# Kernel tuning notes

Hardware: AMD Instinct MI355X
Metric: run time of the kernel (lower is better)

## Reference

```python
import jax, jax.numpy as jnp
import numpy as np
from functools import partial

CONF_THRESH = 0.01
NMS_THRESH = 0.45
TOP_K = 200


def setup_inputs() -> dict:
    key = jax.random.key(0)
    k1, k2, k3 = jax.random.split(key, 3)
    B, N, C = 256, 8732, 21
    loc_data = jax.random.normal(k1, (B, N, 4), dtype=jnp.float32)
    conf_data = jax.random.normal(k2, (B, N, C), dtype=jnp.float32)
    dbox_list = jax.random.uniform(k3, (N, 4), dtype=jnp.float32)
    return {"loc_data": loc_data, "conf_data": conf_data, "dbox_list": dbox_list}


def decode(loc, dbox):
    # loc, dbox: (N, 4). Faithful to torch decode: variances 0.1 / 0.2.
    cxcy = dbox[:, :2] + loc[:, :2] * 0.1 * dbox[:, 2:]
    wh = dbox[:, 2:] * jnp.exp(loc[:, 2:] * 0.2)
    xymin = cxcy - wh / 2.0
    xymax = xymin + wh
    return jnp.concatenate([xymin, xymax], axis=1)  # (N,4) xmin,ymin,xmax,ymax


def nms_single(boxes, scores):
    # boxes: (N,4), scores: (N,). Returns (TOP_K, 5) rows [conf, x1, y1, x2, y2]
    # compacted to the front in descending-score keep order (matches torch output[i,cl,:count]).
    masked = jnp.where(scores > CONF_THRESH, scores, -1.0)
    top_scores, top_idx = jax.lax.top_k(masked, TOP_K)
    b = boxes[top_idx]  # (TOP_K, 4)
    x1, y1, x2, y2 = b[:, 0], b[:, 1], b[:, 2], b[:, 3]
    area = (x2 - x1) * (y2 - y1)
    valid = top_scores > CONF_THRESH

    def body(i, state):
        suppressed, keep = state
        active = jnp.logical_not(suppressed[i])
        keep = keep.at[i].set(active)
        # Faithful to source: all four coords are clamped with min=coord[i]
        # (i.e. elementwise max), including x2/y2 -- reproducing the original math.
        xx1 = jnp.maximum(x1, x1[i])
        yy1 = jnp.maximum(y1, y1[i])
        xx2 = jnp.maximum(x2, x2[i])
        yy2 = jnp.maximum(y2, y2[i])
        inter = (xx2 - xx1) * (yy2 - yy1)
        union = area - inter + area[i]
        iou = inter / union
        sup_new = jnp.logical_and(active, iou > NMS_THRESH)
        sup_new = sup_new.at[i].set(False)
        return jnp.logical_or(suppressed, sup_new), keep

    suppressed0 = jnp.logical_not(valid)
    keep0 = jnp.zeros((TOP_K,), dtype=bool)
    suppressed, keep = jax.lax.fori_loop(0, TOP_K, body, (suppressed0, keep0))

    rows = jnp.concatenate([top_scores[:, None], b], axis=1)  # (TOP_K, 5)
    rows = jnp.where(keep[:, None], rows, 0.0)
    dest = jnp.where(keep, jnp.cumsum(keep) - 1, TOP_K)  # dump slot TOP_K
    out = jnp.zeros((TOP_K + 1, 5), dtype=boxes.dtype).at[dest].set(rows)
    return out[:TOP_K]


def reference(loc_data, conf_data, dbox_list):
    # loc_data: (B, 8732, 4); conf_data: (B, 8732, 21); dbox_list: (8732, 4)
    conf = jax.nn.softmax(conf_data, axis=-1)          # (B, N, C)
    conf_preds = jnp.transpose(conf, (0, 2, 1))        # (B, C, N)
    decoded = jax.vmap(decode, in_axes=(0, None))(loc_data, dbox_list)  # (B, N, 4)
    per_class = jax.vmap(lambda bx, sc: jax.vmap(lambda s: nms_single(bx, s))(sc))(
        decoded, conf_preds
    )  # (B, C, TOP_K, 5)
    # class 0 is background and is skipped in the torch loop -> zeros
    return per_class.at[:, 0].set(0.0)
```

## Files before the change

kernel.cpp:

```cpp
#include <hip/hip_runtime.h>
#include <cstdint>

#pragma clang fp contract(off)

#define TPB 256
typedef unsigned int uint32;
typedef unsigned short u16;
typedef unsigned long long u64;

constexpr int BB = 256;
constexpr int NN = 8732;
constexpr int CC = 21;
constexpr int KK = 200;
constexpr int CH = (NN + TPB - 1) / TPB;
constexpr uint32 KBIAS = 0x3C23D70Au;

__device__ __forceinline__ double fexp(double a) {
  const double L2E = 1.4426950408889634074;
  const double SHIFT = 6755399441055744.0;
  double t = __builtin_fma(a, L2E, SHIFT);
  int i = (int)__double_as_longlong(t);
  double n = t - SHIFT;
  double r = __builtin_fma(n, -6.93147180369123816490e-01, a);
  r = __builtin_fma(n, -1.90821492927058770002e-10, r);
  double p = 1.6059043836821614599e-10;
  p = __builtin_fma(p, r, 2.0876756987868098979e-9);
  p = __builtin_fma(p, r, 2.5052108385441718775e-8);
  p = __builtin_fma(p, r, 2.7557319223985890653e-7);
  p = __builtin_fma(p, r, 2.7557319223985890653e-6);
  p = __builtin_fma(p, r, 2.4801587301587301587e-5);
  p = __builtin_fma(p, r, 1.9841269841269841270e-4);
  p = __builtin_fma(p, r, 1.3888888888888888889e-3);
  p = __builtin_fma(p, r, 8.3333333333333333333e-3);
  p = __builtin_fma(p, r, 4.1666666666666666667e-2);
  p = __builtin_fma(p, r, 1.6666666666666666667e-1);
  p = __builtin_fma(p, r, 0.5);
  p = __builtin_fma(p, r, 1.0);
  p = __builtin_fma(p, r, 1.0);
  return p * __longlong_as_double((long long)(1023 + i) << 52);
}

struct NmsS {
  alignas(16) float bx1[256];
  alignas(16) float by1[256];
  alignas(16) float bx2[256];
  alignas(16) float by2[256];
  alignas(16) float barea[256];
  alignas(16) float bscore[256];
  alignas(16) u64 mask[KK][4];
  u64 kept[4];
};
struct SmemT {
  union alignas(16) UU {
    u16 s16[NN];
    NmsS nms;
  } u;
  uint32 hist[512];
  alignas(16) u64 cand[256];
  uint32 sc4[4];
  uint32 bc[3];
  uint32 slot;
};
static_assert(sizeof(SmemT) <= 22 * 1024, "LDS budget for 7 blocks/CU");

__device__ __forceinline__ uint32 kk_of(float p) {
  return (p > 0.01f) ? (__float_as_uint(p) - KBIAS) : 0u;
}

__device__ __forceinline__ void scan_find(SmemT& sm, uint32 target, int t, int lane, int wv,
                                          uint32& pivot, uint32& cntabove, uint32& pivcnt,
                                          uint32& total) {
  uint32 h0 = sm.hist[2 * t], h1 = sm.hist[2 * t + 1];
  uint32 part = h0 + h1;
  uint32 suf = part;
  for (int off = 1; off < 64; off <<= 1) {
    uint32 v = __shfl_down(suf, off, 64);
    if (lane + off < 64) suf += v;
  }
  if (lane == 0) sm.sc4[wv] = suf;
  __syncthreads();
  uint32 tot = sm.sc4[0] + sm.sc4[1] + sm.sc4[2] + sm.sc4[3];
  uint32 add = 0;
  for (int w = wv + 1; w < 4; ++w) add += sm.sc4[w];
  uint32 mine = suf + add, nxt = mine - part;
  if (mine >= target && nxt < target) {
    uint32 acc = nxt + h1;
    if (acc >= target) { sm.bc[0] = 2u * t + 1u; sm.bc[1] = nxt; sm.bc[2] = h1; }
    else               { sm.bc[0] = 2u * t;      sm.bc[1] = acc; sm.bc[2] = h0; }
  }
  __syncthreads();
  sm.hist[2 * t] = 0u;
  sm.hist[2 * t + 1] = 0u;
  pivot = sm.bc[0];
  cntabove = sm.bc[1];
  pivcnt = sm.bc[2];
  total = tot;
  __syncthreads();
}

template <int MODE>
__global__ __launch_bounds__(TPB, 6) void prep_kernel(const float* __restrict__ conf,
                                                      float* __restrict__ probsT,
                                                      double2* __restrict__ ms) {
  __shared__ float tile[TPB * CC];
  const int blk = blockIdx.x;
  const int b = blockIdx.y;
  const int n0 = blk * TPB;
  const int cnt = (NN - n0 < TPB) ? (NN - n0) : TPB;
  const size_t base = ((size_t)b * NN + n0) * CC;
  if (cnt == TPB) {
    const float4* s4 = (const float4*)(conf + base);
    float4* t4 = (float4*)tile;
    for (int i = threadIdx.x; i < (TPB * CC) / 4; i += TPB) t4[i] = s4[i];
  } else {
    for (int i = threadIdx.x; i < cnt * CC; i += TPB) tile[i] = conf[base + i];
  }
  __syncthreads();
  if (threadIdx.x >= cnt) return;
  const int n = n0 + threadIdx.x;
  const float* cp = tile + threadIdx.x * CC;
  float mx = cp[0];
#pragma unroll
  for (int j = 1; j < CC; ++j) mx = fmaxf(mx, cp[j]);
  const double mxd = (double)mx;

  if (MODE == 0) {
    double es1[CC - 1];
    double S = fexp((double)cp[0] - mxd);
#pragma unroll
    for (int j = 1; j < CC; ++j) {
      es1[j - 1] = fexp((double)cp[j] - mxd);
      S += es1[j - 1];
    }
    const double Sinv = 1.0 / S;
    bool slow = false;
    float* op = probsT + (size_t)b * 20 * NN + n;
#pragma unroll
    for (int c2 = 1; c2 < CC; ++c2) {
      double ph = es1[c2 - 1] * Sinv;
      uint32 low29 = (uint32)__double_as_longlong(ph) & 0x1FFFFFFFu;
      uint32 dist = (low29 > 0x10000000u) ? (low29 - 0x10000000u) : (0x10000000u - low29);
      slow = slow || (dist <= 320u) || (ph < 1e-30);
      op[(size_t)(c2 - 1) * NN] = (float)ph;
    }
    if (__builtin_expect(slow, 0)) {
      double es2[CC];
      double S2 = 0.0;
      for (int j = 0; j < CC; ++j) {
        es2[j] = exp((double)cp[j] - mxd);
        S2 += es2[j];
      }
      double Si2 = 1.0 / S2;
      for (int c2 = 1; c2 < CC; ++c2) op[(size_t)(c2 - 1) * NN] = (float)(es2[c2] * Si2);
    }
  } else {
    double S = 0.0;
#pragma unroll
    for (int j = 0; j < CC; ++j) S += exp((double)cp[j] - mxd);
    ms[(size_t)b * NN + n] = make_double2(mxd, 1.0 / S);
  }
}

template <int MODE>
__device__ __forceinline__ float prob_one(const float* __restrict__ prow,
                                          const float* __restrict__ conf,
                                          const double2* __restrict__ ms,
                                          int b, int c, int n) {
  if (MODE == 0) {
    return prow[n];
  } else if (MODE == 1) {
    double2 mv = ms[(size_t)b * NN + n];
    float x = conf[((size_t)b * NN + n) * CC + c];
    return (float)(exp((double)x - mv.x) * mv.y);
  } else {
    const float* cp = conf + ((size_t)b * NN + n) * CC;
    float mx = cp[0];
    for (int j = 1; j < CC; ++j) mx = fmaxf(mx, cp[j]);
    double S = 0.0, ec = 0.0;
    for (int j = 0; j < CC; ++j) {
      double e = exp((double)cp[j] - (double)mx);
      S += e;
      if (j == c) ec = e;
    }
    return (float)(ec * (1.0 / S));
  }
}

__device__ __forceinline__ void mask_unit(NmsS& nm, int r, int wq, int jcnt) {
  const double MD = 0x1.CCCCCDp-2;
  const float xi1 = nm.bx1[r], yi1 = nm.by1[r];
  const float xi2 = nm.bx2[r], yi2 = nm.by2[r];
  const float ai = nm.barea[r];
  const int jbeg = wq * 64;
  u64 w = 0;
#pragma unroll 4
  for (int j0 = jbeg; j0 < jbeg + jcnt; j0 += 4) {
    const float4 q1 = *(const float4*)&nm.bx1[j0];
    const float4 q2 = *(const float4*)&nm.by1[j0];
    const float4 q3 = *(const float4*)&nm.bx2[j0];
    const float4 q4 = *(const float4*)&nm.by2[j0];
    const float4 qa = *(const float4*)&nm.barea[j0];
    const float a1[4] = {q1.x, q1.y, q1.z, q1.w};
    const float a2[4] = {q2.x, q2.y, q2.z, q2.w};
    const float a3[4] = {q3.x, q3.y, q3.z, q3.w};
    const float a4[4] = {q4.x, q4.y, q4.z, q4.w};
    const float aa[4] = {qa.x, qa.y, qa.z, qa.w};
#pragma unroll
    for (int e = 0; e < 4; ++e) {
      const int j = j0 + e;
      float xx1 = fmaxf(a1[e], xi1);
      float yy1 = fmaxf(a2[e], yi1);
      float xx2 = fmaxf(a3[e], xi2);
      float yy2 = fmaxf(a4[e], yi2);
      float inter = (xx2 - xx1) * (yy2 - yy1);
      float uni = (aa[e] - inter) + ai;
      bool sup = (uni > 0.0f) ? ((double)inter > MD * (double)uni)
                              : (uni == 0.0f && inter > 0.0f);
      if (sup && j > r) w |= 1ull << (j & 63);
    }
  }
  nm.mask[r][wq] = w;
}

template <int MODE>
__global__ __launch_bounds__(TPB, 7) void nms_kernel(
    const float* __restrict__ probsT, const float* __restrict__ conf,
    const double2* __restrict__ ms, const float* __restrict__ loc,
    const float* __restrict__ dbox, float* __restrict__ out) {
  __shared__ SmemT sm;
  const int t = threadIdx.x;
  const int lane = t & 63;
  const int wv = t >> 6;
  const int tb = blockIdx.x;
  const int xcd = tb & 7;
  const int s0i = tb >> 3;
  const int bi = s0i / CC;
  const int c = s0i - bi * CC;
  const int b = bi * 8 + xcd;
  const size_t outbase = (size_t)(b * CC + c) * KK * 5;

  if (c == 0) {
    for (int i = t; i < KK * 5; i += TPB) out[outbase + i] = 0.0f;
    return;
  }
  const float* prow = (MODE == 0) ? probsT + ((size_t)b * 20 + (c - 1)) * NN : nullptr;

  sm.hist[t] = 0u;
  sm.hist[t + 256] = 0u;
  if (t == 0) sm.slot = 0u;
  __syncthreads();

  if (MODE == 0) {
    const float4* p4 = (const float4*)prow;
    for (int i = t; i < NN / 4; i += TPB) {
      float4 p = p4[i];
      uint32 k0 = kk_of(p.x), k1 = kk_of(p.y), k2 = kk_of(p.z), k3 = kk_of(p.w);
      uint32 s0 = k0 ? (k0 >> 10) + 1u : 0u;
      uint32 s1 = k1 ? (k1 >> 10) + 1u : 0u;
      uint32 s2 = k2 ? (k2 >> 10) + 1u : 0u;
      uint32 s3 = k3 ? (k3 >> 10) + 1u : 0u;
      ((u64*)sm.u.s16)[i] = (u64)s0 | ((u64)s1 << 16) | ((u64)s2 << 32) | ((u64)s3 << 48);
      if (s0) atomicAdd(&sm.hist[s0 >> 8], 1u);
      if (s1) atomicAdd(&sm.hist[s1 >> 8], 1u);
      if (s2) atomicAdd(&sm.hist[s2 >> 8], 1u);
      if (s3) atomicAdd(&sm.hist[s3 >> 8], 1u);
    }
  } else {
    for (int n = t; n < NN; n += TPB) {
      uint32 k = kk_of(prob_one<MODE>(prow, conf, ms, b, c, n));
      uint32 s = k ? (k >> 10) + 1u : 0u;
      sm.u.s16[n] = (u16)s;
      if (s) atomicAdd(&sm.hist[s >> 8], 1u);
    }
  }
  __syncthreads();
  uint32 P0, cg0, pc0, total;
  scan_find(sm, (uint32)KK, t, lane, wv, P0, cg0, pc0, total);

  const bool few = total < (uint32)KK;
  uint32 P16, cgA = 0, eqc = 0, ncand;
  if (!few) {
    for (int i = t; i < NN / 2; i += TPB) {
      uint32 w = ((const uint32*)sm.u.s16)[i];
      uint32 a = w & 0xFFFFu, bq = w >> 16;
      if ((a >> 8) == P0) atomicAdd(&sm.hist[a & 0xFFu], 1u);
      if ((bq >> 8) == P0) atomicAdd(&sm.hist[bq & 0xFFu], 1u);
    }
    __syncthreads();
    uint32 P1, cg1, pc1, tot1;
    scan_find(sm, (uint32)KK - cg0, t, lane, wv, P1, cg1, pc1, tot1);
    P16 = (P0 << 8) | P1;
    cgA = cg0 + cg1;
    eqc = pc1;
    ncand = cgA + eqc;
  } else {
    P16 = 1u;
    ncand = total;
  }

  u64 val = 0;
  if (ncand <= 256u) {
    sm.cand[t] = 0ull;
    __syncthreads();
    for (int i = t; i < NN / 2; i += TPB) {
      uint32 w = ((const uint32*)sm.u.s16)[i];
      uint32 a = w & 0xFFFFu, bq = w >> 16;
      if (a >= P16) { uint32 s = atomicAdd(&sm.slot, 1u); sm.cand[s] = (u64)(2 * i); }
      if (bq >= P16) { uint32 s = atomicAdd(&sm.slot, 1u); sm.cand[s] = (u64)(2 * i + 1); }
    }
    __syncthreads();
    if (few) {
      const int base = t * CH;
      const int endn = (base + CH < NN) ? (base + CH) : NN;
      uint32 cz = 0;
      for (int n = base; n < endn; ++n) cz += (sm.u.s16[n] == 0);
      uint32 incl = cz;
      for (int off = 1; off < 64; off <<= 1) {
        uint32 v = __shfl_up(incl, off, 64);
        if (lane >= off) incl += v;
      }
      if (lane == 63) sm.sc4[wv] = incl;
      __syncthreads();
      uint32 add = 0;
      for (int w2 = 0; w2 < wv; ++w2) add += sm.sc4[w2];
      uint32 g = add + incl - cz;
      const uint32 npad = (uint32)KK - ncand;
      if (cz && g < npad) {
        for (int n = base; n < endn && g < npad; ++n)
          if (sm.u.s16[n] == 0) { sm.cand[ncand + g] = (u64)n; ++g; }
      }
      __syncthreads();
    }
    const uint32 ntot = few ? (uint32)KK : ncand;
    if (t < (int)ntot) {
      uint32 idx = (uint32)sm.cand[t];
      uint32 k = (t < (int)ncand) ? kk_of(prob_one<MODE>(prow, conf, ms, b, c, (int)idx)) : 0u;
      val = ((u64)k << 32) | (uint32)(~idx);
    }
  } else {
    const uint32 BK = P16 - 1u;
    const uint32 tgt = (uint32)KK - cgA;
    for (int n = t; n < NN; n += TPB) {
      uint32 k = kk_of(prob_one<MODE>(prow, conf, ms, b, c, n));
      if (k && (k >> 10) == BK) atomicAdd(&sm.hist[(k >> 5) & 31u], 1u);
    }
    __syncthreads();
    uint32 q0, d0, px, tx;
    scan_find(sm, tgt, t, lane, wv, q0, d0, px, tx);
    for (int n = t; n < NN; n += TPB) {
      uint32 k = kk_of(prob_one<MODE>(prow, conf, ms, b, c, n));
      if (k && (k >> 5) == ((BK << 5) | q0)) atomicAdd(&sm.hist[k & 31u], 1u);
    }
    __syncthreads();
    uint32 q1, d1, py, ty;
    scan_find(sm, tgt - d0, t, lane, wv, q1, d1, py, ty);
    const uint32 T = (BK << 10) | (q0 << 5) | q1;
    const uint32 cnt_gt = cgA + d0 + d1;
    const uint32 m_need = (uint32)KK - cnt_gt;
    sm.cand[t] = 0ull;
    if (t == 0) sm.slot = 0u;
    __syncthreads();
    const int base = t * CH;
    const int endn = (base + CH < NN) ? (base + CH) : NN;
    uint32 cnteq = 0;
    for (int n = base; n < endn; ++n) {
      uint32 k = kk_of(prob_one<MODE>(prow, conf, ms, b, c, n));
      if (k > T) {
        uint32 s = atomicAdd(&sm.slot, 1u);
        sm.cand[s] = ((u64)k << 32) | (uint32)(~(uint32)n);
      }
      cnteq += (k == T);
    }
    uint32 incl = cnteq;
    for (int off = 1; off < 64; off <<= 1) {
      uint32 v = __shfl_up(incl, off, 64);
      if (lane >= off) incl += v;
    }
    if (lane == 63) sm.sc4[wv] = incl;
    __syncthreads();
    uint32 add = 0;
    for (int w2 = 0; w2 < wv; ++w2) add += sm.sc4[w2];
    uint32 g = add + incl - cnteq;
    if (cnteq && g < m_need) {
      for (int n = base; n < endn && g < m_need; ++n) {
        uint32 k = kk_of(prob_one<MODE>(prow, conf, ms, b, c, n));
        if (k == T) {
          sm.cand[cnt_gt + g] = ((u64)T << 32) | (uint32)(~(uint32)n);
          ++g;
        }
      }
    }
    __syncthreads();
    val = sm.cand[t];
  }

  for (int kk = 2; kk <= 256; kk <<= 1) {
    for (int j = kk >> 1; j > 0; j >>= 1) {
      u64 other;
      if (j >= 64) {
        __syncthreads();
        sm.cand[t] = val;
        __syncthreads();
        other = sm.cand[t ^ j];
      } else {
        other = __shfl_xor((unsigned long long)val, j, 64);
      }
      const bool takeMax = ((t & kk) == 0) == ((t & j) == 0);
      val = takeMax ? (val > other ? val : other) : (val < other ? val : other);
    }
  }
  __syncthreads();

  if (t < KK) {
    uint32 k32 = (uint32)(val >> 32);
    uint32 idx = ~((uint32)val);
    bool valid = k32 != 0u;
    float score = valid ? __uint_as_float(k32 + KBIAS) : -1.0f;
    const float4 lc = ((const float4*)loc)[(size_t)b * NN + idx];
    const float4 db = ((const float4*)dbox)[idx];
    float cx = db.x + (lc.x * 0.1f) * db.z;
    float cy = db.y + (lc.y * 0.1f) * db.w;
    float w_ = db.z * (float)exp((double)(lc.z * 0.2f));
    float h_ = db.w * (float)exp((double)(lc.w * 0.2f));
    float x1 = cx - w_ * 0.5f;
    float y1 = cy - h_ * 0.5f;
    float x2 = x1 + w_;
    float y2 = y1 + h_;
    sm.u.nms.bx1[t] = x1;
    sm.u.nms.by1[t] = y1;
    sm.u.nms.bx2[t] = x2;
    sm.u.nms.by2[t] = y2;
    sm.u.nms.barea[t] = (x2 - x1) * (y2 - y1);
    sm.u.nms.bscore[t] = score;
  } else {
    sm.u.nms.bscore[t] = -1.0f;
  }
  __syncthreads();

  {
    int u1 = t;
    int wqa = (u1 < 64) ? 0 : (u1 < 192) ? 1 : 2;
    int ra = (u1 < 64) ? u1 : (u1 < 192) ? (u1 - 64) : (u1 - 192);
    mask_unit(sm.u.nms, ra, wqa, 64);
    if (t >= 128) {
      int rb = (t - 128) + 64;
      mask_unit(sm.u.nms, rb, 2, 64);
    }
    if (t < KK) mask_unit(sm.u.nms, t, 3, 8);
  }
  __syncthreads();

  if (wv == 0) {
    u64 s0 = __ballot(!(sm.u.nms.bscore[lane] > 0.01f));
    u64 s1 = __ballot(!(sm.u.nms.bscore[64 + lane] > 0.01f));
    u64 s2 = __ballot(!(sm.u.nms.bscore[128 + lane] > 0.01f));
    u64 s3 = __ballot(!(sm.u.nms.bscore[192 + lane] > 0.01f)) | ~0xFFull;
    u64 k0 = 0, k1 = 0, k2 = 0, k3 = 0;
    const u64(*M)[4] = sm.u.nms.mask;
    u64 pre[8][4];
#pragma unroll
    for (int s = 0; s < 8; ++s) {
      pre[s][0] = M[s][0]; pre[s][1] = M[s][1];
      pre[s][2] = M[s][2]; pre[s][3] = M[s][3];
    }
#define WALK_BLOCK(SW, KW, CNT, IBASE)                                   \
  _Pragma("unroll 8")                                                    \
  for (int ii = 0; ii < (CNT); ++ii) {                                   \
    const int s = ii & 7;                                                \
    u64 c0 = pre[s][0], c1 = pre[s][1], c2 = pre[s][2], c3 = pre[s][3];  \
    const int inext = (IBASE) + ii + 8;                                  \
    pre[s][0] = M[inext][0]; pre[s][1] = M[inext][1];                    \
    pre[s][2] = M[inext][2]; pre[s][3] = M[inext][3];                    \
    u64 bm = 1ull << ii;                                                 \
    if (!((SW) & bm)) {                                                  \
      (KW) |= bm;                                                        \
      s0 |= c0; s1 |= c1; s2 |= c2; s3 |= c3;                            \
    }                                                                    \
  }
    WALK_BLOCK(s0, k0, 64, 0)
    WALK_BLOCK(s1, k1, 64, 64)
    WALK_BLOCK(s2, k2, 64, 128)
    WALK_BLOCK(s3, k3, 8, 192)
#undef WALK_BLOCK
    if (lane == 0) {
      sm.u.nms.kept[0] = k0; sm.u.nms.kept[1] = k1;
      sm.u.nms.kept[2] = k2; sm.u.nms.kept[3] = k3;
    }
  } else {
    float4 z4 = make_float4(0.f, 0.f, 0.f, 0.f);
    float4* o4 = (float4*)(out + outbase);
    for (int i = t - 64; i < (KK * 5) / 4; i += 192) o4[i] = z4;
  }
  __syncthreads();

  if (t < KK) {
    const u64 K0 = sm.u.nms.kept[0], K1 = sm.u.nms.kept[1];
    const u64 K2 = sm.u.nms.kept[2], K3 = sm.u.nms.kept[3];
    const int w = t >> 6;
    const int bit = t & 63;
    u64 kw = (w == 0) ? K0 : (w == 1) ? K1 : (w == 2) ? K2 : K3;
    bool kp = (kw >> bit) & 1ull;
    if (kp) {
      u64 lowm = (bit == 0) ? 0ull : (~0ull >> (64 - bit));
      int d = __popcll(kw & lowm);
      if (w > 0) d += __popcll(K0);
      if (w > 1) d += __popcll(K1);
      if (w > 2) d += __popcll(K2);
      float* o = out + outbase + (size_t)d * 5;
      o[0] = sm.u.nms.bscore[t];
      o[1] = sm.u.nms.bx1[t];
      o[2] = sm.u.nms.by1[t];
      o[3] = sm.u.nms.bx2[t];
      o[4] = sm.u.nms.by2[t];
    }
  }
}

extern "C" void kernel_launch(void* const* d_in, const int* in_sizes, int n_in,
                              void* d_out, int out_size, void* d_ws, size_t ws_size,
                              hipStream_t stream) {
  (void)in_sizes; (void)n_in; (void)out_size;
  const float* loc = (const float*)d_in[0];
  const float* conf = (const float*)d_in[1];
  const float* dbox = (const float*)d_in[2];
  float* out = (float*)d_out;

  const size_t needA = (size_t)BB * 20 * NN * sizeof(float);
  const size_t needB = (size_t)BB * NN * sizeof(double2);
  dim3 blk(TPB);
  dim3 g1((NN + TPB - 1) / TPB, BB);
  const int g2 = BB * CC;

  if (ws_size >= needA) {
    float* probsT = (float*)d_ws;
    prep_kernel<0><<<g1, blk, 0, stream>>>(conf, probsT, nullptr);
    nms_kernel<0><<<g2, blk, 0, stream>>>(probsT, conf, nullptr, loc, dbox, out);
  } else if (ws_size >= needB) {
    double2* msp = (double2*)d_ws;
    prep_kernel<1><<<g1, blk, 0, stream>>>(conf, nullptr, msp);
    nms_kernel<1><<<g2, blk, 0, stream>>>(nullptr, conf, msp, loc, dbox, out);
  } else {
    nms_kernel<2><<<g2, blk, 0, stream>>>(nullptr, conf, nullptr, loc, dbox, out);
  }
}
```

Before: 493.4 us.

## Rebalance triangular NMS mask work into 32-bit chunks and scalarize greedy walk

```diff
diff --git a/kernel.cpp b/kernel.cpp
--- a/kernel.cpp
+++ b/kernel.cpp
@@ -40,6 +40,20 @@
   return p * __longlong_as_double((long long)(1023 + i) << 52);
 }
 
+__device__ __forceinline__ float exp_f32_exact(float xf) {
+  double v = fexp((double)xf);
+  uint32 low29 = (uint32)__double_as_longlong(v) & 0x1FFFFFFFu;
+  uint32 dist = (low29 > 0x10000000u) ? (low29 - 0x10000000u) : (0x10000000u - low29);
+  if (__builtin_expect(dist <= 65536u, 0)) v = exp((double)xf);
+  return (float)v;
+}
+
+__device__ __forceinline__ u64 rfl64(u64 v) {
+  uint32 lo = (uint32)__builtin_amdgcn_readfirstlane((int)(uint32)v);
+  uint32 hi = (uint32)__builtin_amdgcn_readfirstlane((int)(uint32)(v >> 32));
+  return ((u64)hi << 32) | lo;
+}
+
 struct NmsS {
   alignas(16) float bx1[256];
   alignas(16) float by1[256];
@@ -99,7 +113,7 @@
 }
 
 template <int MODE>
-__global__ __launch_bounds__(TPB, 6) void prep_kernel(const float* __restrict__ conf,
+__global__ __launch_bounds__(TPB, 5) void prep_kernel(const float* __restrict__ conf,
                                                       float* __restrict__ probsT,
                                                       double2* __restrict__ ms) {
   __shared__ float tile[TPB * CC];
@@ -186,15 +200,15 @@
   }
 }
 
-__device__ __forceinline__ void mask_unit(NmsS& nm, int r, int wq, int jcnt) {
+__device__ __forceinline__ void mask_unit32(NmsS& nm, int r, int c) {
   const double MD = 0x1.CCCCCDp-2;
   const float xi1 = nm.bx1[r], yi1 = nm.by1[r];
   const float xi2 = nm.bx2[r], yi2 = nm.by2[r];
   const float ai = nm.barea[r];
-  const int jbeg = wq * 64;
-  u64 w = 0;
-#pragma unroll 4
-  for (int j0 = jbeg; j0 < jbeg + jcnt; j0 += 4) {
+  const int jbeg = c * 32;
+  uint32 w = 0;
+#pragma unroll
+  for (int j0 = jbeg; j0 < jbeg + 32; j0 += 4) {
     const float4 q1 = *(const float4*)&nm.bx1[j0];
     const float4 q2 = *(const float4*)&nm.by1[j0];
     const float4 q3 = *(const float4*)&nm.bx2[j0];
@@ -216,10 +230,45 @@
       float uni = (aa[e] - inter) + ai;
       bool sup = (uni > 0.0f) ? ((double)inter > MD * (double)uni)
                               : (uni == 0.0f && inter > 0.0f);
-      if (sup && j > r) w |= 1ull << (j & 63);
-    }
-  }
-  nm.mask[r][wq] = w;
+      if (sup && j > r) w |= 1u << (j & 31);
+    }
+  }
+  ((uint32*)&nm.mask[r][0])[c] = w;
+}
+
+__device__ __forceinline__ void mask_unit_short(NmsS& nm, int r) {
+  const double MD = 0x1.CCCCCDp-2;
+  const float xi1 = nm.bx1[r], yi1 = nm.by1[r];
+  const float xi2 = nm.bx2[r], yi2 = nm.by2[r];
+  const float ai = nm.barea[r];
+  uint32 w = 0;
+#pragma unroll
+  for (int j0 = 192; j0 < 200; j0 += 4) {
+    const float4 q1 = *(const float4*)&nm.bx1[j0];
+    const float4 q2 = *(const float4*)&nm.by1[j0];
+    const float4 q3 = *(const float4*)&nm.bx2[j0];
+    const float4 q4 = *(const float4*)&nm.by2[j0];
+    const float4 qa = *(const float4*)&nm.barea[j0];
+    const float a1[4] = {q1.x, q1.y, q1.z, q1.w};
+    const float a2[4] = {q2.x, q2.y, q2.z, q2.w};
+    const float a3[4] = {q3.x, q3.y, q3.z, q3.w};
+    const float a4[4] = {q4.x, q4.y, q4.z, q4.w};
+    const float aa[4] = {qa.x, qa.y, qa.z, qa.w};
+#pragma unroll
+    for (int e = 0; e < 4; ++e) {
+      const int j = j0 + e;
+      float xx1 = fmaxf(a1[e], xi1);
+      float yy1 = fmaxf(a2[e], yi1);
+      float xx2 = fmaxf(a3[e], xi2);
+      float yy2 = fmaxf(a4[e], yi2);
+      float inter = (xx2 - xx1) * (yy2 - yy1);
+      float uni = (aa[e] - inter) + ai;
+      bool sup = (uni > 0.0f) ? ((double)inter > MD * (double)uni)
+                              : (uni == 0.0f && inter > 0.0f);
+      if (sup && j > r) w |= 1u << (j & 31);
+    }
+  }
+  ((uint32*)&nm.mask[r][0])[6] = w;
 }
 
 template <int MODE>
@@ -420,8 +469,8 @@
     const float4 db = ((const float4*)dbox)[idx];
     float cx = db.x + (lc.x * 0.1f) * db.z;
     float cy = db.y + (lc.y * 0.1f) * db.w;
-    float w_ = db.z * (float)exp((double)(lc.z * 0.2f));
-    float h_ = db.w * (float)exp((double)(lc.w * 0.2f));
+    float w_ = db.z * exp_f32_exact(lc.z * 0.2f);
+    float h_ = db.w * exp_f32_exact(lc.w * 0.2f);
     float x1 = cx - w_ * 0.5f;
     float y1 = cy - h_ * 0.5f;
     float x2 = x1 + w_;
@@ -438,15 +487,24 @@
   __syncthreads();
 
   {
-    int u1 = t;
-    int wqa = (u1 < 64) ? 0 : (u1 < 192) ? 1 : 2;
-    int ra = (u1 < 64) ? u1 : (u1 < 192) ? (u1 - 64) : (u1 - 192);
-    mask_unit(sm.u.nms, ra, wqa, 64);
-    if (t >= 128) {
-      int rb = (t - 128) + 64;
-      mask_unit(sm.u.nms, rb, 2, 64);
-    }
-    if (t < KK) mask_unit(sm.u.nms, t, 3, 8);
+    {
+      int u = t;
+      int cq = (u >= 192) ? ((u >= 480) ? 5 : ((u >= 320) ? 4 : 3))
+                          : ((u >= 96) ? 2 : ((u >= 32) ? 1 : 0));
+      int off = 16 * cq * (cq + 1);
+      mask_unit32(sm.u.nms, u - off, cq);
+    }
+    {
+      int u = 256 + t;
+      int cq = (u >= 480) ? 5 : ((u >= 320) ? 4 : 3);
+      int off = 16 * cq * (cq + 1);
+      mask_unit32(sm.u.nms, u - off, cq);
+    }
+    if (t < 160) {
+      int u = 512 + t;
+      mask_unit32(sm.u.nms, u - 480, 5);
+    }
+    if (t < KK) mask_unit_short(sm.u.nms, t);
   }
   __syncthreads();
 
@@ -457,20 +515,23 @@
     u64 s3 = __ballot(!(sm.u.nms.bscore[192 + lane] > 0.01f)) | ~0xFFull;
     u64 k0 = 0, k1 = 0, k2 = 0, k3 = 0;
     const u64(*M)[4] = sm.u.nms.mask;
-    u64 pre[8][4];
-#pragma unroll
-    for (int s = 0; s < 8; ++s) {
-      pre[s][0] = M[s][0]; pre[s][1] = M[s][1];
-      pre[s][2] = M[s][2]; pre[s][3] = M[s][3];
+    u64 pre[4][4];
+#pragma unroll
+    for (int s = 0; s < 4; ++s) {
+      ulonglong2 a = ((const ulonglong2*)M[s])[0];
+      ulonglong2 bb = ((const ulonglong2*)M[s])[1];
+      pre[s][0] = a.x; pre[s][1] = a.y; pre[s][2] = bb.x; pre[s][3] = bb.y;
     }
 #define WALK_BLOCK(SW, KW, CNT, IBASE)                                   \
-  _Pragma("unroll 8")                                                    \
+  _Pragma("unroll 4")                                                    \
   for (int ii = 0; ii < (CNT); ++ii) {                                   \
-    const int s = ii & 7;                                                \
-    u64 c0 = pre[s][0], c1 = pre[s][1], c2 = pre[s][2], c3 = pre[s][3];  \
-    const int inext = (IBASE) + ii + 8;                                  \
-    pre[s][0] = M[inext][0]; pre[s][1] = M[inext][1];                    \
-    pre[s][2] = M[inext][2]; pre[s][3] = M[inext][3];                    \
+    const int s = ii & 3;                                                \
+    u64 c0 = rfl64(pre[s][0]), c1 = rfl64(pre[s][1]);                    \
+    u64 c2 = rfl64(pre[s][2]), c3 = rfl64(pre[s][3]);                    \
+    const int inext = (IBASE) + ii + 4;                                  \
+    ulonglong2 na = ((const ulonglong2*)M[inext])[0];                    \
+    ulonglong2 nb = ((const ulonglong2*)M[inext])[1];                    \
+    pre[s][0] = na.x; pre[s][1] = na.y; pre[s][2] = nb.x; pre[s][3] = nb.y; \
     u64 bm = 1ull << ii;                                                 \
     if (!((SW) & bm)) {                                                  \
       (KW) |= bm;                                                        \
```

Measured after the change: 466.8 us. 1.06x faster.
